# Kernel optimization log

Hardware: AMD Instinct MI355X
Metric: run time of the kernel (lower is better)

## Reference

```python
import jax, jax.numpy as jnp
import numpy as np

EPS = 1e-6


def _cosine(mem, keys):
    # mem: [B,N,C], keys: [B,C,R] -> [B,N,R]
    dot = jnp.einsum('bnc,bcr->bnr', mem, keys)
    mn = jnp.linalg.norm(mem, axis=2, keepdims=True)      # [B,N,1]
    kn = jnp.linalg.norm(keys, axis=1, keepdims=True)     # [B,1,R]
    return dot / (mn * kn + EPS)


def setup_inputs() -> dict:
    B, N, C, R = 8, 2048, 256, 4
    key = jax.random.key(0)
    ks = jax.random.split(key, 16)
    return {
        'memory': jax.random.normal(ks[0], (B, N, C), jnp.float32),
        'link': jax.random.uniform(ks[1], (B, N, N), jnp.float32),
        'usage': jax.random.uniform(ks[2], (B, N), jnp.float32),
        'read_weights': jax.random.uniform(ks[3], (B, N, R), jnp.float32),
        'write_weight_prev': jax.random.uniform(ks[4], (B, N), jnp.float32),
        'precedence': jax.random.uniform(ks[5], (B, N), jnp.float32),
        'read_keys': jax.random.normal(ks[6], (B, C, R), jnp.float32),
        'read_strengths': jax.random.uniform(ks[7], (B, R), jnp.float32),
        'write_key': jax.random.normal(ks[8], (B, C), jnp.float32),
        'write_strength': jax.random.uniform(ks[9], (B, 1), jnp.float32),
        'free_gates': jax.random.uniform(ks[10], (B, R), jnp.float32),
        'allocation_gate': jax.random.uniform(ks[11], (B, 1), jnp.float32),
        'write_gate': jax.random.uniform(ks[12], (B, 1), jnp.float32),
        'write_vector': jax.random.normal(ks[13], (B, C), jnp.float32),
        'erase_vector': jax.random.uniform(ks[14], (B, C), jnp.float32),
        'read_modes': jax.random.uniform(ks[15], (B, 3, R), jnp.float32),
    }


def reference(memory, link, usage, read_weights, write_weight_prev, precedence,
              read_keys, read_strengths, write_key, write_strength, free_gates,
              allocation_gate, write_gate, write_vector, erase_vector, read_modes):
    B, N, C = memory.shape
    # --- usage update: psi retention from free gates ---
    psi = jnp.prod(1.0 - free_gates[:, None, :] * read_weights, axis=2)  # [B,N]
    u = (usage + write_weight_prev - usage * write_weight_prev) * psi
    # --- allocation weighting (sorted exclusive cumprod) ---
    order = jnp.argsort(u, axis=1)                                     # ascending usage
    u_sorted = jnp.take_along_axis(u, order, axis=1)
    excl = jnp.concatenate([jnp.ones_like(u_sorted[:, :1]),
                            jnp.cumprod(u_sorted[:, :-1], axis=1)], axis=1)
    a_sorted = (1.0 - u_sorted) * excl
    inv = jnp.argsort(order, axis=1)
    alloc = jnp.take_along_axis(a_sorted, inv, axis=1)                 # [B,N]
    # --- write weighting ---
    phi_w = _cosine(memory, write_key[:, :, None])[:, :, 0]            # [B,N]
    cw = jax.nn.softmax(phi_w * write_strength, axis=1)
    ww = write_gate * (allocation_gate * alloc + (1.0 - allocation_gate) * cw)  # [B,N]
    # --- memory write (erase + add) ---
    mem_new = memory * (1.0 - ww[:, :, None] * erase_vector[:, None, :]) \
              + ww[:, :, None] * write_vector[:, None, :]
    # --- precedence + link matrix ---
    prec_new = (1.0 - jnp.sum(ww, axis=1, keepdims=True)) * precedence + ww
    link_new = (1.0 - ww[:, :, None] - ww[:, None, :]) * link \
               + ww[:, :, None] * precedence[:, None, :]
    link_new = link_new * (1.0 - jnp.eye(N, dtype=link.dtype))[None]
    # --- directional weightings ---
    fwd = jnp.einsum('bij,bjr->bir', link_new, read_weights)           # [B,N,R]
    bwd = jnp.einsum('bji,bjr->bir', link_new, read_weights)
    # --- content read weighting on updated memory ---
    phi_r = _cosine(mem_new, read_keys)                                # [B,N,R]
    cr = jax.nn.softmax(phi_r * read_strengths[:, None, :], axis=1)
    rw_new = read_modes[:, 0][:, None, :] * bwd \
             + read_modes[:, 1][:, None, :] * cr \
             + read_modes[:, 2][:, None, :] * fwd                      # [B,N,R]
    # --- read vectors ---
    read_vectors = jnp.einsum('bnc,bnr->bcr', mem_new, rw_new)         # [B,C,R]
    return read_vectors
```

## Files before the change

### kernel.cpp

```cpp
#include <hip/hip_runtime.h>
#include <math.h>

#define EPS 1e-6f
constexpr int B = 8, N = 2048, C = 256, R = 4;

__device__ __forceinline__ float wred_sum(float v) {
  for (int d = 32; d; d >>= 1) v += __shfl_xor(v, d, 64);
  return v;
}

__device__ __forceinline__ float ww_inline(float sw, float al, float dw,
                                           float agv, float wgv) {
  return wgv * (agv * al + (1.f - agv) * (expf(sw) / dw));
}

__global__ __launch_bounds__(1024) void k_pre(const float* __restrict__ usage,
    const float* __restrict__ wwp, const float* __restrict__ fg,
    const float* __restrict__ rw, const float* __restrict__ mem,
    const float* __restrict__ wk, const float* __restrict__ wstr,
    float* __restrict__ alloc_, float* __restrict__ sw_, float* __restrict__ denw) {
  __shared__ float2 ulg[N];
  __shared__ float Sp[16][64];
  __shared__ float eacc[16];
  int blk = blockIdx.x;
  int t = threadIdx.x;
  if (blk < 256) {
    int b = blk >> 5, chunk = blk & 31;
    float gx = fg[b * R + 0], gy = fg[b * R + 1], gz = fg[b * R + 2], gw2 = fg[b * R + 3];
    for (int e = t; e < N; e += 1024) {
      float4 r4 = *(const float4*)&rw[(size_t)(b * N + e) * R];
      float psi = (1.f - gx * r4.x) * (1.f - gy * r4.y) * (1.f - gz * r4.z) * (1.f - gw2 * r4.w);
      float us = usage[b * N + e], w = wwp[b * N + e];
      float u = (us + w - us * w) * psi;
      ulg[e] = make_float2(u, log2f(u));
    }
    __syncthreads();
    int i = chunk * 64 + (t & 63);
    int jseg = t >> 6;
    float ui = ulg[i].x;
    float S = 0.f;
    int j0 = jseg * 128;
    #pragma unroll 4
    for (int jj = 0; jj < 128; jj++) {
      int j = j0 + jj;
      float2 v = ulg[j];
      bool sel = (v.x < ui) || (v.x == ui && j < i);
      S += sel ? v.y : 0.f;
    }
    Sp[jseg][t & 63] = S;
    __syncthreads();
    if (t < 64) {
      float tot = 0.f;
      #pragma unroll
      for (int s = 0; s < 16; s++) tot += Sp[s][t];
      int ii = chunk * 64 + t;
      alloc_[b * N + ii] = (1.f - ulg[ii].x) * exp2f(tot);
    }
  } else {
    int wv = t >> 6, lane = t & 63;
    int gw = (blk - 256) * 16 + wv;
    int b = gw >> 11, n = gw & (N - 1);
    float4 m4 = *(const float4*)&mem[(size_t)(b * N + n) * C + lane * 4];
    float4 k4 = *(const float4*)&wk[b * C + lane * 4];
    float dot = m4.x * k4.x + m4.y * k4.y + m4.z * k4.z + m4.w * k4.w;
    float nrm = m4.x * m4.x + m4.y * m4.y + m4.z * m4.z + m4.w * m4.w;
    float knr = k4.x * k4.x + k4.y * k4.y + k4.z * k4.z + k4.w * k4.w;
    for (int d = 32; d; d >>= 1) {
      dot += __shfl_xor(dot, d, 64);
      nrm += __shfl_xor(nrm, d, 64);
      knr += __shfl_xor(knr, d, 64);
    }
    if (lane == 0) {
      float phi = dot / (sqrtf(nrm) * sqrtf(knr) + EPS);
      float swv = phi * wstr[b];
      sw_[b * N + n] = swv;
      eacc[wv] = expf(swv);
    }
    __syncthreads();
    if (t == 0) {
      float s = 0.f;
      #pragma unroll
      for (int i = 0; i < 16; i++) s += eacc[i];
      atomicAdd(&denw[b], s);
    }
  }
}

__global__ __launch_bounds__(512) void k_cw(const float* __restrict__ rw,
    const float* __restrict__ sw_, const float* __restrict__ alloc_,
    const float* __restrict__ denw, const float* __restrict__ ag,
    const float* __restrict__ wg, const float* __restrict__ prec,
    float* __restrict__ cwg, float* __restrict__ ST_) {
  __shared__ float red8[8][8];
  int blk = blockIdx.x, t = threadIdx.x;
  int b = blk >> 2, seg = blk & 3;
  int n = seg * 512 + t;
  int lane = t & 63, wv = t >> 6;
  float agv = ag[b], wgv = wg[b], dw = denw[b];
  float4 r4 = *(const float4*)&rw[(size_t)(b * N + n) * R];
  float w = ww_inline(sw_[b * N + n], alloc_[b * N + n], dw, agv, wgv);
  float pc = prec[b * N + n];
  float4 lo = { r4.x, r4.y, r4.z, r4.w };
  float4 hi = { w * r4.x, w * r4.y, w * r4.z, w * r4.w };
  *(float4*)&cwg[(size_t)(b * N + n) * 8] = lo;
  *(float4*)&cwg[(size_t)(b * N + n) * 8 + 4] = hi;
  float a[8] = { pc * r4.x, pc * r4.y, pc * r4.z, pc * r4.w,
                 w * r4.x,  w * r4.y,  w * r4.z,  w * r4.w };
  #pragma unroll
  for (int r = 0; r < 8; r++) a[r] = wred_sum(a[r]);
  if (lane == 0) {
    #pragma unroll
    for (int r = 0; r < 8; r++) red8[wv][r] = a[r];
  }
  __syncthreads();
  if (t < 8) {
    float s = 0.f;
    #pragma unroll
    for (int i = 0; i < 8; i++) s += red8[i][t];
    atomicAdd(&ST_[b * 8 + t], s);
  }
}

__global__ __launch_bounds__(512) void k_mid(const float* __restrict__ link,
    const float* __restrict__ rw, const float* __restrict__ sw_,
    const float* __restrict__ alloc_, const float* __restrict__ denw,
    const float* __restrict__ ag, const float* __restrict__ wg,
    const float* __restrict__ mem, const float* __restrict__ rk,
    const float* __restrict__ ev, const float* __restrict__ wvec,
    const float* __restrict__ rs, const float* __restrict__ cwg,
    float* __restrict__ t_, float* __restrict__ upart, float* __restrict__ sr_,
    float* __restrict__ denr) {
  __shared__ float tile[2][64][65];
  __shared__ float cwt[2][64][8];
  __shared__ float ri8l[64][8];
  __shared__ float tred[8][64][9];
  __shared__ float eacc[8][4];
  const int blk = blockIdx.x;
  const int t = threadIdx.x;
  const int lane = t & 63, wv = t >> 6;
  if (blk < 256) {
    const int b = blk >> 5;
    const int strip = blk & 31;
    const int i0 = strip * 64;
    const int jb = t * 4;
    const int lr = t >> 3, lc = (t & 7) * 8;
    const int li = t & 63, seg = t >> 6;
    ri8l[t >> 3][t & 7] = cwg[(size_t)(b * N + i0) * 8 + t];
    float tacc[8] = { 0, 0, 0, 0, 0, 0, 0, 0 };
    float uacc[4][8];
    #pragma unroll
    for (int k = 0; k < 4; k++) {
      #pragma unroll
      for (int r = 0; r < 8; r++) uacc[k][r] = 0.f;
    }
    const float* lsrc = link + (size_t)(b * N + i0 + lr) * N + lc;
    {
      float4 pa = *(const float4*)lsrc;
      float4 pb = *(const float4*)(lsrc + 4);
      float cwreg = cwg[(size_t)(b * N) * 8 + t];
      tile[0][lr][lc + 0] = pa.x; tile[0][lr][lc + 1] = pa.y;
      tile[0][lr][lc + 2] = pa.z; tile[0][lr][lc + 3] = pa.w;
      tile[0][lr][lc + 4] = pb.x; tile[0][lr][lc + 5] = pb.y;
      tile[0][lr][lc + 6] = pb.z; tile[0][lr][lc + 7] = pb.w;
      cwt[0][t >> 3][t & 7] = cwreg;
    }
    __syncthreads();
    for (int T = 0; T < 32; T++) {
      const int cur = T & 1;
      float4 pa, pb;
      float cwreg;
      if (T < 31) {
        pa = *(const float4*)(lsrc + (size_t)(T + 1) * 64);
        pb = *(const float4*)(lsrc + (size_t)(T + 1) * 64 + 4);
        cwreg = cwg[(size_t)(b * N + (T + 1) * 64) * 8 + t];
      }
      #pragma unroll
      for (int jj = 0; jj < 8; jj++) {
        int j = seg * 8 + jj;
        float lv = tile[cur][li][j];
        float4 c0 = *(const float4*)&cwt[cur][j][0];
        float4 c1 = *(const float4*)&cwt[cur][j][4];
        tacc[0] = fmaf(lv, c0.x, tacc[0]);
        tacc[1] = fmaf(lv, c0.y, tacc[1]);
        tacc[2] = fmaf(lv, c0.z, tacc[2]);
        tacc[3] = fmaf(lv, c0.w, tacc[3]);
        tacc[4] = fmaf(lv, c1.x, tacc[4]);
        tacc[5] = fmaf(lv, c1.y, tacc[5]);
        tacc[6] = fmaf(lv, c1.z, tacc[6]);
        tacc[7] = fmaf(lv, c1.w, tacc[7]);
      }
      if (T < 31) {
        const int nb = cur ^ 1;
        tile[nb][lr][lc + 0] = pa.x; tile[nb][lr][lc + 1] = pa.y;
        tile[nb][lr][lc + 2] = pa.z; tile[nb][lr][lc + 3] = pa.w;
        tile[nb][lr][lc + 4] = pb.x; tile[nb][lr][lc + 5] = pb.y;
        tile[nb][lr][lc + 6] = pb.z; tile[nb][lr][lc + 7] = pb.w;
        cwt[nb][t >> 3][t & 7] = cwreg;
      }
      __syncthreads();
    }
    for (int ii = 0; ii < 64; ii += 4) {
      float4 La[4];
      #pragma unroll
      for (int m = 0; m < 4; m++)
        La[m] = *(const float4*)(link + (size_t)(b * N + i0 + ii + m) * N + jb);
      #pragma unroll
      for (int m = 0; m < 4; m++) {
        float lv[4] = { La[m].x, La[m].y, La[m].z, La[m].w };
        #pragma unroll
        for (int k = 0; k < 4; k++) {
          #pragma unroll
          for (int r = 0; r < 8; r++)
            uacc[k][r] = fmaf(lv[k], ri8l[ii + m][r], uacc[k][r]);
        }
      }
    }
    #pragma unroll
    for (int r = 0; r < 8; r++) tred[seg][li][r] = tacc[r];
    __syncthreads();
    {
      const int i = t & 63, rr = t >> 6;
      float s = 0.f;
      #pragma unroll
      for (int sg = 0; sg < 8; sg++) s += tred[sg][i][rr];
      t_[((size_t)(b * 8 + rr)) * N + i0 + i] = s;
    }
    float* ub = upart + ((size_t)(b * 32 + strip) * 8) * N;
    #pragma unroll
    for (int r = 0; r < 8; r++) {
      float4 v = { uacc[0][r], uacc[1][r], uacc[2][r], uacc[3][r] };
      *(float4*)(ub + (size_t)r * N + jb) = v;
    }
  } else {
    int gw = (blk - 256) * 8 + wv;
    int b = gw >> 11, n = gw & (N - 1);
    const float agv = ag[b], wgv = wg[b], dw = denw[b];
    float w = ww_inline(sw_[b * N + n], alloc_[b * N + n], dw, agv, wgv);
    int c0i = lane * 4;
    float4 m4 = *(const float4*)&mem[(size_t)(b * N + n) * C + c0i];
    float4 e4 = *(const float4*)&ev[b * C + c0i];
    float4 v4 = *(const float4*)&wvec[b * C + c0i];
    float mn[4] = { m4.x * (1.f - w * e4.x) + w * v4.x,
                    m4.y * (1.f - w * e4.y) + w * v4.y,
                    m4.z * (1.f - w * e4.z) + w * v4.z,
                    m4.w * (1.f - w * e4.w) + w * v4.w };
    float dot[4] = { 0, 0, 0, 0 };
    float kn[4] = { 0, 0, 0, 0 };
    float nrm = 0.f;
    #pragma unroll
    for (int ci = 0; ci < 4; ci++) {
      float4 k4 = *(const float4*)&rk[(size_t)(b * C + c0i + ci) * R];
      dot[0] = fmaf(mn[ci], k4.x, dot[0]);
      dot[1] = fmaf(mn[ci], k4.y, dot[1]);
      dot[2] = fmaf(mn[ci], k4.z, dot[2]);
      dot[3] = fmaf(mn[ci], k4.w, dot[3]);
      kn[0] = fmaf(k4.x, k4.x, kn[0]);
      kn[1] = fmaf(k4.y, k4.y, kn[1]);
      kn[2] = fmaf(k4.z, k4.z, kn[2]);
      kn[3] = fmaf(k4.w, k4.w, kn[3]);
      nrm = fmaf(mn[ci], mn[ci], nrm);
    }
    for (int d = 32; d; d >>= 1) {
      dot[0] += __shfl_xor(dot[0], d, 64);
      dot[1] += __shfl_xor(dot[1], d, 64);
      dot[2] += __shfl_xor(dot[2], d, 64);
      dot[3] += __shfl_xor(dot[3], d, 64);
      kn[0] += __shfl_xor(kn[0], d, 64);
      kn[1] += __shfl_xor(kn[1], d, 64);
      kn[2] += __shfl_xor(kn[2], d, 64);
      kn[3] += __shfl_xor(kn[3], d, 64);
      nrm += __shfl_xor(nrm, d, 64);
    }
    if (lane == 0) {
      float mnorm = sqrtf(nrm);
      #pragma unroll
      for (int r = 0; r < 4; r++) {
        float phi = dot[r] / (mnorm * sqrtf(kn[r]) + EPS);
        float sv = phi * rs[b * R + r];
        sr_[(size_t)(b * R + r) * N + n] = sv;
        eacc[wv][r] = expf(sv);
      }
    }
    __syncthreads();
    if (t < 4) {
      float s = 0.f;
      #pragma unroll
      for (int i = 0; i < 8; i++) s += eacc[i][t];
      atomicAdd(&denr[b * R + t], s);
    }
  }
}

__global__ __launch_bounds__(256) void k_combread(const float* __restrict__ link,
    const float* __restrict__ sw_, const float* __restrict__ alloc_,
    const float* __restrict__ denw, const float* __restrict__ denr,
    const float* __restrict__ ag, const float* __restrict__ wg,
    const float* __restrict__ prec, const float* __restrict__ rw,
    const float* __restrict__ t_, const float* __restrict__ upart,
    const float* __restrict__ sr_, const float* __restrict__ ST_,
    const float* __restrict__ modes, const float* __restrict__ mem,
    const float* __restrict__ ev, const float* __restrict__ wvec,
    float* __restrict__ part_) {
  __shared__ float dgl[64], wloc[64], rwnl[4][64];
  __shared__ float red[4][64][4][4];
  const int blk = blockIdx.x;
  const int b = blk >> 5, chunk = blk & 31;
  const int n0 = chunk * 64;
  const int t = threadIdx.x;
  const int nl = t & 63, r = t >> 6;
  const int n = n0 + nl;
  const float agv = ag[b], wgv = wg[b], dw = denw[b];
  float u1 = 0.f, u2 = 0.f;
  const float* up = upart + ((size_t)(b * 32) * 8) * N;
  #pragma unroll 8
  for (int s = 0; s < 32; s++) {
    const float* p = up + ((size_t)s * 8) * N;
    u1 += p[(size_t)r * N + n];
    u2 += p[(size_t)(4 + r) * N + n];
  }
  float pc = prec[b * N + n];
  if (r == 0) {
    float w = ww_inline(sw_[b * N + n], alloc_[b * N + n], dw, agv, wgv);
    float L = link[((size_t)(b * N + n)) * N + n];
    dgl[nl] = (1.f - 2.f * w) * L + w * pc;
    wloc[nl] = w;
  }
  __syncthreads();
  {
    float w = wloc[nl], Dg = dgl[nl];
    float t1 = t_[(size_t)(b * 8 + r) * N + n];
    float t2 = t_[(size_t)(b * 8 + 4 + r) * N + n];
    float sv = sr_[(size_t)(b * R + r) * N + n];
    float cr = expf(sv) / denr[b * R + r];
    float rv = rw[(size_t)(b * N + n) * R + r];
    float S = ST_[b * 8 + r], T = ST_[b * 8 + 4 + r];
    float m0 = modes[(b * 3 + 0) * R + r], m1 = modes[(b * 3 + 1) * R + r],
          m2 = modes[(b * 3 + 2) * R + r];
    float fwd = (1.f - w) * t1 - t2 + w * S - Dg * rv;
    float bwd = (1.f - w) * u1 - u2 + pc * T - Dg * rv;
    rwnl[r][nl] = m0 * bwd + m1 * cr + m2 * fwd;
  }
  __syncthreads();
  const int sub = r, cg = nl;
  const int c0 = cg * 4;
  float4 e4 = *(const float4*)&ev[b * C + c0];
  float4 v4 = *(const float4*)&wvec[b * C + c0];
  float acc[4][4];
  #pragma unroll
  for (int ci = 0; ci < 4; ci++) {
    #pragma unroll
    for (int rr = 0; rr < 4; rr++) acc[ci][rr] = 0.f;
  }
  for (int m = 0; m < 16; m++) {
    int row = sub * 16 + m;
    int nn = n0 + row;
    float w = wloc[row];
    float4 m4 = *(const float4*)&mem[(size_t)(b * N + nn) * C + c0];
    float mn[4] = { m4.x * (1.f - w * e4.x) + w * v4.x,
                    m4.y * (1.f - w * e4.y) + w * v4.y,
                    m4.z * (1.f - w * e4.z) + w * v4.z,
                    m4.w * (1.f - w * e4.w) + w * v4.w };
    float rv[4] = { rwnl[0][row], rwnl[1][row], rwnl[2][row], rwnl[3][row] };
    #pragma unroll
    for (int ci = 0; ci < 4; ci++) {
      #pragma unroll
      for (int rr = 0; rr < 4; rr++) acc[ci][rr] = fmaf(mn[ci], rv[rr], acc[ci][rr]);
    }
  }
  #pragma unroll
  for (int ci = 0; ci < 4; ci++) {
    #pragma unroll
    for (int rr = 0; rr < 4; rr++) red[sub][cg][ci][rr] = acc[ci][rr];
  }
  __syncthreads();
  if (sub == 0) {
    #pragma unroll
    for (int ci = 0; ci < 4; ci++) {
      #pragma unroll
      for (int rr = 0; rr < 4; rr++) {
        float s = red[0][cg][ci][rr] + red[1][cg][ci][rr] +
                  red[2][cg][ci][rr] + red[3][cg][ci][rr];
        part_[((size_t)blk * C + (c0 + ci)) * R + rr] = s;
      }
    }
  }
}

__global__ void k_final(const float* __restrict__ part_, float* __restrict__ out) {
  int idx = blockIdx.x * 256 + threadIdx.x;
  if (idx >= B * C * R) return;
  int b = idx / (C * R), cr = idx % (C * R);
  float s = 0.f;
  for (int ch = 0; ch < 32; ch++) s += part_[(size_t)(b * 32 + ch) * C * R + cr];
  out[idx] = s;
}

extern "C" void kernel_launch(void* const* d_in, const int* in_sizes, int n_in,
                              void* d_out, int out_size, void* d_ws, size_t ws_size,
                              hipStream_t stream) {
  const float* mem   = (const float*)d_in[0];
  const float* link  = (const float*)d_in[1];
  const float* usage = (const float*)d_in[2];
  const float* rw    = (const float*)d_in[3];
  const float* wwp   = (const float*)d_in[4];
  const float* prec  = (const float*)d_in[5];
  const float* rk    = (const float*)d_in[6];
  const float* rs    = (const float*)d_in[7];
  const float* wk    = (const float*)d_in[8];
  const float* wstr  = (const float*)d_in[9];
  const float* fg    = (const float*)d_in[10];
  const float* ag    = (const float*)d_in[11];
  const float* wg    = (const float*)d_in[12];
  const float* wvec  = (const float*)d_in[13];
  const float* ev    = (const float*)d_in[14];
  const float* modes = (const float*)d_in[15];
  float* out = (float*)d_out;

  float* W = (float*)d_ws;
  float* denw  = W;
  float* denr  = W + 8;
  float* ST_   = W + 64;
  float* alloc_= W + 128;
  float* sw_   = alloc_ + B * N;
  float* t_    = sw_ + B * N;
  float* sr_   = t_ + B * 8 * N;
  float* part_ = sr_ + B * R * N;
  float* cwg   = part_ + B * 32 * C * R;
  float* upart = cwg + B * N * 8;

  (void)hipMemsetAsync(W, 0, 128 * sizeof(float), stream);
  k_pre<<<256 + (B * N) / 16, 1024, 0, stream>>>(usage, wwp, fg, rw, mem, wk, wstr,
                                                 alloc_, sw_, denw);
  k_cw<<<B * 4, 512, 0, stream>>>(rw, sw_, alloc_, denw, ag, wg, prec, cwg, ST_);
  k_mid<<<256 + (B * N) / 8, 512, 0, stream>>>(link, rw, sw_, alloc_, denw, ag, wg,
                                               mem, rk, ev, wvec, rs, cwg,
                                               t_, upart, sr_, denr);
  k_combread<<<B * 32, 256, 0, stream>>>(link, sw_, alloc_, denw, denr, ag, wg, prec,
                                         rw, t_, upart, sr_, ST_, modes, mem, ev,
                                         wvec, part_);
  k_final<<<(B * C * R) / 256, 256, 0, stream>>>(part_, out);
}
```

Before: 137.5 us.

## Compute link-times-weights product with bf16 MFMA in separate wave-level blocks

The forward link product (link rows times the 8-column weight matrix) moves from a shared-memory tiled FMA loop to per-wave 16x16x32 bf16 MFMA instructions. k_cw now also writes the weights pre-swizzled into MFMA fragment layout. The link matrix is read twice now, once by the new MFMA blocks and once by the existing transpose-product blocks, which no longer share a tile. Converting link and weights to bf16 lowers precision and adds an extra memset and global buffer.

```diff
diff --git a/kernel.cpp b/kernel.cpp
--- a/kernel.cpp
+++ b/kernel.cpp
@@ -3,10 +3,18 @@
 
 #define EPS 1e-6f
 constexpr int B = 8, N = 2048, C = 256, R = 4;
+
+typedef short bf16x8 __attribute__((ext_vector_type(8)));
+typedef float f32x4 __attribute__((ext_vector_type(4)));
 
 __device__ __forceinline__ float wred_sum(float v) {
   for (int d = 32; d; d >>= 1) v += __shfl_xor(v, d, 64);
   return v;
+}
+__device__ __forceinline__ unsigned short f2bf(float f) {
+  unsigned int x = __float_as_uint(f);
+  unsigned int r = x + 0x7FFFu + ((x >> 16) & 1u);
+  return (unsigned short)(r >> 16);
 }
 
 __device__ __forceinline__ float ww_inline(float sw, float al, float dw,
@@ -90,7 +98,8 @@
     const float* __restrict__ sw_, const float* __restrict__ alloc_,
     const float* __restrict__ denw, const float* __restrict__ ag,
     const float* __restrict__ wg, const float* __restrict__ prec,
-    float* __restrict__ cwg, float* __restrict__ ST_) {
+    float* __restrict__ cwg, unsigned short* __restrict__ cwfrag,
+    float* __restrict__ ST_) {
   __shared__ float red8[8][8];
   int blk = blockIdx.x, t = threadIdx.x;
   int b = blk >> 2, seg = blk & 3;
@@ -100,10 +109,14 @@
   float4 r4 = *(const float4*)&rw[(size_t)(b * N + n) * R];
   float w = ww_inline(sw_[b * N + n], alloc_[b * N + n], dw, agv, wgv);
   float pc = prec[b * N + n];
-  float4 lo = { r4.x, r4.y, r4.z, r4.w };
-  float4 hi = { w * r4.x, w * r4.y, w * r4.z, w * r4.w };
-  *(float4*)&cwg[(size_t)(b * N + n) * 8] = lo;
-  *(float4*)&cwg[(size_t)(b * N + n) * 8 + 4] = hi;
+  float vals[8] = { r4.x, r4.y, r4.z, r4.w, w * r4.x, w * r4.y, w * r4.z, w * r4.w };
+  *(float4*)&cwg[(size_t)(b * N + n) * 8] = make_float4(vals[0], vals[1], vals[2], vals[3]);
+  *(float4*)&cwg[(size_t)(b * N + n) * 8 + 4] = make_float4(vals[4], vals[5], vals[6], vals[7]);
+  {
+    size_t base = (((size_t)(b * 64 + (n >> 5))) * 64 + ((n & 31) >> 3) * 16) * 8 + (n & 7);
+    #pragma unroll
+    for (int c = 0; c < 8; c++) cwfrag[base + (size_t)c * 8] = f2bf(vals[c]);
+  }
   float a[8] = { pc * r4.x, pc * r4.y, pc * r4.z, pc * r4.w,
                  w * r4.x,  w * r4.y,  w * r4.z,  w * r4.w };
   #pragma unroll
@@ -128,77 +141,53 @@
     const float* __restrict__ mem, const float* __restrict__ rk,
     const float* __restrict__ ev, const float* __restrict__ wvec,
     const float* __restrict__ rs, const float* __restrict__ cwg,
+    const unsigned short* __restrict__ cwfrag,
     float* __restrict__ t_, float* __restrict__ upart, float* __restrict__ sr_,
     float* __restrict__ denr) {
-  __shared__ float tile[2][64][65];
-  __shared__ float cwt[2][64][8];
   __shared__ float ri8l[64][8];
-  __shared__ float tred[8][64][9];
   __shared__ float eacc[8][4];
   const int blk = blockIdx.x;
   const int t = threadIdx.x;
   const int lane = t & 63, wv = t >> 6;
-  if (blk < 256) {
-    const int b = blk >> 5;
-    const int strip = blk & 31;
+  if (blk < 128) {
+    const int g = blk * 8 + wv;
+    const int b = g >> 7;
+    const int i0 = (g & 127) * 16;
+    f32x4 acc = { 0.f, 0.f, 0.f, 0.f };
+    const float* ap = link + ((size_t)(b * N + i0 + (lane & 15))) * N + ((lane >> 4) * 8);
+    const bf16x8* cfp = (const bf16x8*)cwfrag + (size_t)(b * 64) * 64 + lane;
+    for (int kk = 0; kk < 64; kk++) {
+      float4 a0 = *(const float4*)(ap + kk * 32);
+      float4 a1 = *(const float4*)(ap + kk * 32 + 4);
+      bf16x8 af;
+      af[0] = (short)f2bf(a0.x); af[1] = (short)f2bf(a0.y);
+      af[2] = (short)f2bf(a0.z); af[3] = (short)f2bf(a0.w);
+      af[4] = (short)f2bf(a1.x); af[5] = (short)f2bf(a1.y);
+      af[6] = (short)f2bf(a1.z); af[7] = (short)f2bf(a1.w);
+      bf16x8 bfv = cfp[(size_t)kk * 64];
+      acc = __builtin_amdgcn_mfma_f32_16x16x32_bf16(af, bfv, acc, 0, 0, 0);
+    }
+    const int col = lane & 15;
+    if (col < 8) {
+      const int rbase = (lane >> 4) * 4;
+      #pragma unroll
+      for (int reg = 0; reg < 4; reg++)
+        t_[((size_t)(b * 8 + col)) * N + i0 + rbase + reg] = acc[reg];
+    }
+  } else if (blk < 384) {
+    const int ub = blk - 128;
+    const int b = ub >> 5;
+    const int strip = ub & 31;
     const int i0 = strip * 64;
     const int jb = t * 4;
-    const int lr = t >> 3, lc = (t & 7) * 8;
-    const int li = t & 63, seg = t >> 6;
     ri8l[t >> 3][t & 7] = cwg[(size_t)(b * N + i0) * 8 + t];
-    float tacc[8] = { 0, 0, 0, 0, 0, 0, 0, 0 };
     float uacc[4][8];
     #pragma unroll
     for (int k = 0; k < 4; k++) {
       #pragma unroll
       for (int r = 0; r < 8; r++) uacc[k][r] = 0.f;
     }
-    const float* lsrc = link + (size_t)(b * N + i0 + lr) * N + lc;
-    {
-      float4 pa = *(const float4*)lsrc;
-      float4 pb = *(const float4*)(lsrc + 4);
-      float cwreg = cwg[(size_t)(b * N) * 8 + t];
-      tile[0][lr][lc + 0] = pa.x; tile[0][lr][lc + 1] = pa.y;
-      tile[0][lr][lc + 2] = pa.z; tile[0][lr][lc + 3] = pa.w;
-      tile[0][lr][lc + 4] = pb.x; tile[0][lr][lc + 5] = pb.y;
-      tile[0][lr][lc + 6] = pb.z; tile[0][lr][lc + 7] = pb.w;
-      cwt[0][t >> 3][t & 7] = cwreg;
-    }
     __syncthreads();
-    for (int T = 0; T < 32; T++) {
-      const int cur = T & 1;
-      float4 pa, pb;
-      float cwreg;
-      if (T < 31) {
-        pa = *(const float4*)(lsrc + (size_t)(T + 1) * 64);
-        pb = *(const float4*)(lsrc + (size_t)(T + 1) * 64 + 4);
-        cwreg = cwg[(size_t)(b * N + (T + 1) * 64) * 8 + t];
-      }
-      #pragma unroll
-      for (int jj = 0; jj < 8; jj++) {
-        int j = seg * 8 + jj;
-        float lv = tile[cur][li][j];
-        float4 c0 = *(const float4*)&cwt[cur][j][0];
-        float4 c1 = *(const float4*)&cwt[cur][j][4];
-        tacc[0] = fmaf(lv, c0.x, tacc[0]);
-        tacc[1] = fmaf(lv, c0.y, tacc[1]);
-        tacc[2] = fmaf(lv, c0.z, tacc[2]);
-        tacc[3] = fmaf(lv, c0.w, tacc[3]);
-        tacc[4] = fmaf(lv, c1.x, tacc[4]);
-        tacc[5] = fmaf(lv, c1.y, tacc[5]);
-        tacc[6] = fmaf(lv, c1.z, tacc[6]);
-        tacc[7] = fmaf(lv, c1.w, tacc[7]);
-      }
-      if (T < 31) {
-        const int nb = cur ^ 1;
-        tile[nb][lr][lc + 0] = pa.x; tile[nb][lr][lc + 1] = pa.y;
-        tile[nb][lr][lc + 2] = pa.z; tile[nb][lr][lc + 3] = pa.w;
-        tile[nb][lr][lc + 4] = pb.x; tile[nb][lr][lc + 5] = pb.y;
-        tile[nb][lr][lc + 6] = pb.z; tile[nb][lr][lc + 7] = pb.w;
-        cwt[nb][t >> 3][t & 7] = cwreg;
-      }
-      __syncthreads();
-    }
     for (int ii = 0; ii < 64; ii += 4) {
       float4 La[4];
       #pragma unroll
@@ -215,24 +204,14 @@
         }
       }
     }
-    #pragma unroll
-    for (int r = 0; r < 8; r++) tred[seg][li][r] = tacc[r];
-    __syncthreads();
-    {
-      const int i = t & 63, rr = t >> 6;
-      float s = 0.f;
-      #pragma unroll
-      for (int sg = 0; sg < 8; sg++) s += tred[sg][i][rr];
-      t_[((size_t)(b * 8 + rr)) * N + i0 + i] = s;
-    }
-    float* ub = upart + ((size_t)(b * 32 + strip) * 8) * N;
+    float* ubp = upart + ((size_t)(b * 32 + strip) * 8) * N;
     #pragma unroll
     for (int r = 0; r < 8; r++) {
       float4 v = { uacc[0][r], uacc[1][r], uacc[2][r], uacc[3][r] };
-      *(float4*)(ub + (size_t)r * N + jb) = v;
+      *(float4*)(ubp + (size_t)r * N + jb) = v;
     }
   } else {
-    int gw = (blk - 256) * 8 + wv;
+    int gw = (blk - 384) * 8 + wv;
     int b = gw >> 11, n = gw & (N - 1);
     const float agv = ag[b], wgv = wg[b], dw = denw[b];
     float w = ww_inline(sw_[b * N + n], alloc_[b * N + n], dw, agv, wgv);
@@ -427,14 +406,16 @@
   float* part_ = sr_ + B * R * N;
   float* cwg   = part_ + B * 32 * C * R;
   float* upart = cwg + B * N * 8;
+  unsigned short* cwfrag = (unsigned short*)(upart + (size_t)B * 32 * 8 * N);
 
   (void)hipMemsetAsync(W, 0, 128 * sizeof(float), stream);
+  (void)hipMemsetAsync(cwfrag, 0, (size_t)B * 64 * 64 * 8 * sizeof(unsigned short), stream);
   k_pre<<<256 + (B * N) / 16, 1024, 0, stream>>>(usage, wwp, fg, rw, mem, wk, wstr,
                                                  alloc_, sw_, denw);
-  k_cw<<<B * 4, 512, 0, stream>>>(rw, sw_, alloc_, denw, ag, wg, prec, cwg, ST_);
-  k_mid<<<256 + (B * N) / 8, 512, 0, stream>>>(link, rw, sw_, alloc_, denw, ag, wg,
-                                               mem, rk, ev, wvec, rs, cwg,
-                                               t_, upart, sr_, denr);
+  k_cw<<<B * 4, 512, 0, stream>>>(rw, sw_, alloc_, denw, ag, wg, prec, cwg, cwfrag, ST_);
+  k_mid<<<128 + 256 + (B * N) / 8, 512, 0, stream>>>(link, rw, sw_, alloc_, denw, ag, wg,
+                                                     mem, rk, ev, wvec, rs, cwg, cwfrag,
+                                                     t_, upart, sr_, denr);
   k_combread<<<B * 32, 256, 0, stream>>>(link, sw_, alloc_, denw, denr, ag, wg, prec,
                                          rw, t_, upart, sr_, ST_, modes, mem, ev,
                                          wvec, part_);
```

Measured after the change: 172.5 us. +25.4%, slower.
